# Optimization experiments

Measured on AMD Instinct MI355X. Metric: run time of the kernel, lower is better.

Reference implementation:

```python
import jax, jax.numpy as jnp
import numpy as np

N_HEADS = 12
HIDDEN = 768  # NOTE: d_head == hidden_size in this module (unusual)

def setup_inputs() -> dict:
    key = jax.random.key(0)
    ks = jax.random.split(key, 4)
    b, s = 8, 512
    d3 = 3 * N_HEADS * HIDDEN
    return {
        "x": jax.random.normal(ks[0], (b, s, HIDDEN), dtype=jnp.float32),
        "mask": jnp.zeros((b, 1, 1, s), dtype=jnp.float32),
        "w_qkv": jax.random.normal(ks[1], (d3, HIDDEN), dtype=jnp.float32) * 0.02,
        "b_qkv": jnp.zeros((d3,), dtype=jnp.float32),
        "w_o": jax.random.normal(ks[2], (HIDDEN, N_HEADS * HIDDEN), dtype=jnp.float32) * 0.02,
        "b_o": jnp.zeros((HIDDEN,), dtype=jnp.float32),
    }

def reference(x, mask, w_qkv, b_qkv, w_o, b_o):
    b, s, _ = x.shape
    nh = N_HEADS * HIDDEN
    qkv = x @ w_qkv.T + b_qkv                      # (b, s, 3*n*h)
    q, k, v = jnp.split(qkv, 3, axis=-1)           # each (b, s, n*h)
    def heads(t):
        return t.reshape(b, s, N_HEADS, HIDDEN).transpose(0, 2, 1, 3)  # (b, n, s, h)
    q, k, v = heads(q), heads(k), heads(v)
    scale = 1.0 / np.sqrt(HIDDEN).astype(np.float32)
    scores = jnp.einsum('bnqh,bnkh->bnqk', q, k) * scale  # (b, n, s_q, s_k)
    scores = scores + mask                         # additive mask broadcast
    a = jax.nn.softmax(scores, axis=-1)
    av = jnp.einsum('bnqk,bnkh->bnqh', a, v)       # (b, n, s, h)
    h = av.transpose(0, 2, 1, 3).reshape(b, s, nh) # (b, s, n*h)
    return h @ w_o.T + b_o                         # (b, s, hidden)
```

## Files before the change

### kernel.cpp

```cpp
#include <hip/hip_runtime.h>
#include <hip/hip_bf16.h>
#include <stdint.h>

#define AS1 __attribute__((address_space(1)))
#define AS3 __attribute__((address_space(3)))

typedef __attribute__((ext_vector_type(8))) __bf16 bf16x8;
typedef __attribute__((ext_vector_type(4))) float f32x4;
typedef unsigned short u16;
typedef __attribute__((ext_vector_type(8))) unsigned short u16x8;

#define B_    8
#define S_    512
#define NH_   12
#define HD_   768
#define NHD_  (NH_*HD_)
#define D3_   (3*NHD_)
#define QKLD_ (2*NHD_)
#define QK_SCALE 0.03608439182435161f

__device__ __forceinline__ u16 f2bf(float x) {
  union { float f; unsigned u; } a; a.f = x;
  unsigned r = a.u + 0x7fffu + ((a.u >> 16) & 1u);
  return (u16)(r >> 16);
}
__device__ __forceinline__ float bf2f(u16 x) {
  union { unsigned u; float f; } a; a.u = ((unsigned)x) << 16; return a.f;
}
__device__ __forceinline__ uint2 pack4(float a, float b, float c, float d) {
  uint2 r;
  asm("v_cvt_pk_bf16_f32 %0, %1, %2" : "=v"(r.x) : "v"(a), "v"(b));
  asm("v_cvt_pk_bf16_f32 %0, %1, %2" : "=v"(r.y) : "v"(c), "v"(d));
  return r;
}

__device__ __forceinline__ void gload16(const void* g, void* l) {
  __builtin_amdgcn_global_load_lds((const AS1 void*)g, (AS3 void*)l, 16, 0, 0);
}

struct GP {
  const u16* A;
  const u16* B;
  long sAb, sAn, sBb, sBn;
  void* o0; void* o2;
  const float* bias;
  int mMask, mShift, zPerX;
};

template<int MODE, int LDA, int LDB, int KK>
__global__ __launch_bounds__(256)
void gemm_bt(GP p) {
  __shared__ __align__(16) char smem[32768];
  const int tid  = threadIdx.x;
  const int wave = tid >> 6, lane = tid & 63;
  const int wr = wave >> 1, wc = wave & 1;

  int m_idx, n_idx, z;
  if constexpr (MODE == 0) {
    m_idx = blockIdx.y; n_idx = blockIdx.x; z = 0;
  } else {
    const int bid = blockIdx.x;
    const int xcd = bid & 7, loc = bid >> 3;
    if constexpr (MODE == 1) {
      int inner;
      if (p.zPerX) { inner = loc & 15; z = xcd * p.zPerX + (loc >> 4); }
      else         { inner = bid & 15; z = bid >> 4; }
      m_idx = inner >> 2; n_idx = inner & 3;
    } else if constexpr (MODE == 2) {
      int inner;
      if (p.zPerX) { inner = loc % 24; z = xcd * p.zPerX + loc / 24; }
      else         { inner = bid % 24; z = bid / 24; }
      m_idx = inner / 6; n_idx = inner - (inner / 6) * 6;
    } else {
      m_idx = loc & p.mMask;
      n_idx = (xcd & 1) * 3 + (loc >> p.mShift);
      z = xcd >> 1;
    }
  }
  const int bm0 = m_idx * 128, bn0 = n_idx * 128;
  const int zb  = z / NH_, zn = z - zb * NH_;

  const u16* A  = p.A + zb * p.sAb + zn * p.sAn;
  const u16* Bm = p.B + zb * p.sBb + zn * p.sBn;

  f32x4 acc[4][4];
  const f32x4 zero4 = {0.f, 0.f, 0.f, 0.f};
#pragma unroll
  for (int i = 0; i < 4; ++i)
#pragma unroll
    for (int j = 0; j < 4; ++j) acc[i][j] = zero4;

  const int scolsw = ((lane & 7) ^ (lane >> 3)) * 8;
  const u16* gA = A  + (size_t)(bm0 + wave*8 + (lane>>3)) * LDA + scolsw;
  const u16* gB = Bm + (size_t)(bn0 + wave*8 + (lane>>3)) * LDB + scolsw;
  char* ldsA = smem;
  char* ldsB = smem + 16384;
  char* stA  = ldsA + wave*1024;
  char* stB  = ldsB + wave*1024;

  const int aRow = (wr*64 + (lane&15)) * 128;
  const int bRow = (wc*64 + (lane&15)) * 128;
  const int csw  = lane & 7;
  const int cOff0 = (((lane>>4)    ) ^ csw) << 4;
  const int cOff1 = ((4 + (lane>>4)) ^ csw) << 4;

  for (int k0 = 0; k0 < KK; k0 += 64) {
#pragma unroll
    for (int i = 0; i < 4; ++i) {
      gload16(gA + (size_t)i*32*LDA, stA + i*4096);
      gload16(gB + (size_t)i*32*LDB, stB + i*4096);
    }
    gA += 64; gB += 64;
    __syncthreads();
#pragma unroll
    for (int kk = 0; kk < 2; ++kk) {
      const int cOff = kk ? cOff1 : cOff0;
      bf16x8 av[4], bv[4];
#pragma unroll
      for (int i = 0; i < 4; ++i)
        av[i] = *(const bf16x8*)(ldsA + aRow + i*2048 + cOff);
#pragma unroll
      for (int j = 0; j < 4; ++j)
        bv[j] = *(const bf16x8*)(ldsB + bRow + j*2048 + cOff);
#pragma unroll
      for (int i = 0; i < 4; ++i)
#pragma unroll
        for (int j = 0; j < 4; ++j)
          acc[i][j] = __builtin_amdgcn_mfma_f32_16x16x32_bf16(bv[j], av[i], acc[i][j], 0, 0, 0);
    }
    __syncthreads();
  }

  const int mBase = bm0 + wr*64 + (lane & 15);
  const int nBase = bn0 + wc*64 + ((lane >> 4) << 2);
#pragma unroll
  for (int i = 0; i < 4; ++i) {
    const int m = mBase + i*16;
#pragma unroll
    for (int j = 0; j < 4; ++j) {
      const int n = nBase + j*16;
      const f32x4 v = acc[i][j];
      if constexpr (MODE == 0) {
        const float4 b4 = *(const float4*)(p.bias + n);
        if (bn0 < QKLD_) {
          *(uint2*)((u16*)p.o0 + (long)m * QKLD_ + n) =
              pack4(v[0]+b4.x, v[1]+b4.y, v[2]+b4.z, v[3]+b4.w);
        } else {
          const int vcol = n - QKLD_;
          const int nh = vcol / HD_;
          const int h  = vcol - nh * HD_;
          u16* vb = (u16*)p.o2 + (long)((m >> 9) * NH_ + nh) * (S_*HD_)
                    + (long)h * S_ + (m & 511);
          vb[0]    = f2bf(v[0]+b4.x);
          vb[512]  = f2bf(v[1]+b4.y);
          vb[1024] = f2bf(v[2]+b4.z);
          vb[1536] = f2bf(v[3]+b4.w);
        }
      } else if constexpr (MODE == 1) {
        *(uint2*)((u16*)p.o0 + (long)z*S_*S_ + (long)m*S_ + n) =
            pack4(v[0]*QK_SCALE, v[1]*QK_SCALE, v[2]*QK_SCALE, v[3]*QK_SCALE);
      } else if constexpr (MODE == 2) {
        *(uint2*)((u16*)p.o0 + (long)(zb*S_ + m)*QKLD_ + zn*HD_ + n) =
            pack4(v[0], v[1], v[2], v[3]);
      } else {
        const long rowsTot = (long)(p.mMask + 1) * 128;
        *(float4*)((float*)p.o0 + ((long)z * rowsTot + m) * HD_ + n) =
            *(const float4*)&v;
      }
    }
  }
}

__global__ __launch_bounds__(256)
void softmax_rows(u16* __restrict__ SP, const float* __restrict__ maskc) {
  const int wave = threadIdx.x >> 6, lane = threadIdx.x & 63;
  const int rid = blockIdx.x * 4 + wave;
  const int z = rid >> 9;
  const int b = z / NH_;
  const u16x8 sv = *(const u16x8*)(SP + (size_t)rid * S_ + lane*8);
  const float* mrow = maskc + (size_t)b * S_;
  float vals[8];
  float m = -3.4e38f;
#pragma unroll
  for (int j = 0; j < 8; ++j) {
    vals[j] = bf2f(sv[j]) + mrow[lane*8 + j];
    m = fmaxf(m, vals[j]);
  }
#pragma unroll
  for (int o = 32; o > 0; o >>= 1) m = fmaxf(m, __shfl_xor(m, o));
  float sum = 0.f;
#pragma unroll
  for (int j = 0; j < 8; ++j) { vals[j] = __expf(vals[j] - m); sum += vals[j]; }
#pragma unroll
  for (int o = 32; o > 0; o >>= 1) sum += __shfl_xor(sum, o);
  const float inv = 1.0f / sum;
  u16x8 pv;
#pragma unroll
  for (int j = 0; j < 8; ++j) pv[j] = f2bf(vals[j] * inv);
  *(u16x8*)(SP + (size_t)rid * S_ + lane*8) = pv;
}

__global__ __launch_bounds__(256)
void cvt_bf16(const float4* __restrict__ in, ushort4* __restrict__ out, int n4) {
  const int i = blockIdx.x * 256 + threadIdx.x;
  if (i >= n4) return;
  const float4 v = in[i];
  ushort4 o;
  o.x = f2bf(v.x); o.y = f2bf(v.y); o.z = f2bf(v.z); o.w = f2bf(v.w);
  out[i] = o;
}

__global__ __launch_bounds__(256)
void combine_out(const float4* __restrict__ part, const float* __restrict__ b,
                 float4* __restrict__ out, int n4) {
  const int i = blockIdx.x * 256 + threadIdx.x;
  if (i >= n4) return;
  const float4 a0 = part[i];
  const float4 a1 = part[i + (size_t)n4];
  const float4 a2 = part[i + (size_t)2*n4];
  const float4 a3 = part[i + (size_t)3*n4];
  const int c = (i * 4) % HD_;
  float4 o;
  o.x = a0.x + a1.x + a2.x + a3.x + b[c];
  o.y = a0.y + a1.y + a2.y + a3.y + b[c+1];
  o.z = a0.z + a1.z + a2.z + a3.z + b[c+2];
  o.w = a0.w + a1.w + a2.w + a3.w + b[c+3];
  out[i] = o;
}

extern "C" void kernel_launch(void* const* d_in, const int* in_sizes, int n_in,
                              void* d_out, int out_size, void* d_ws, size_t ws_size,
                              hipStream_t stream) {
  const float* x     = (const float*)d_in[0];
  const float* mask  = (const float*)d_in[1];
  const float* w_qkv = (const float*)d_in[2];
  const float* b_qkv = (const float*)d_in[3];
  const float* w_o   = (const float*)d_in[4];
  const float* b_o   = (const float*)d_in[5];
  float* out = (float*)d_out;

  int bc = 0;
  for (int c = 8; c >= 1; c >>= 1)
    if (56623104UL + (unsigned long)c*35389440UL <= ws_size) { bc = c; break; }
  if (bc == 0) return;

  char* ws = (char*)d_ws;
  u16* wqb = (u16*)(ws);
  u16* wob = (u16*)(ws + 42467328L);
  u16* xb  = (u16*)(ws + 56623104L);
  long off = 56623104L + (long)bc*786432L;
  u16* QKn = (u16*)(ws + off);  off += (long)bc*18874368L;
  u16* Vt  = (u16*)(ws + off);  off += (long)bc*9437184L;
  u16* SP  = (u16*)(ws + off);
  u16* H   = QKn;
  float* Part = (float*)SP;

  cvt_bf16<<<dim3(D3_*HD_/4/256), dim3(256), 0, stream>>>((const float4*)w_qkv, (ushort4*)wqb, D3_*HD_/4);
  cvt_bf16<<<dim3(HD_*NHD_/4/256), dim3(256), 0, stream>>>((const float4*)w_o, (ushort4*)wob, HD_*NHD_/4);

  const int nchunks = B_ / bc;
  const int rows_c = bc * S_;
  const int zc = bc * NH_;
  const int mT = rows_c / 128;
  const int mShift = __builtin_ctz(mT);
  const int zPerX = (zc % 8 == 0) ? zc / 8 : 0;

  for (int c = 0; c < nchunks; ++c) {
    const long row0 = (long)c * rows_c;

    cvt_bf16<<<dim3(rows_c*HD_/4/256), dim3(256), 0, stream>>>(
        (const float4*)(x + row0*HD_), (ushort4*)xb, rows_c*HD_/4);

    GP p1; p1.A = xb; p1.B = wqb;
    p1.sAb = 0; p1.sAn = 0; p1.sBb = 0; p1.sBn = 0;
    p1.o0 = QKn; p1.o2 = Vt; p1.bias = b_qkv;
    p1.mMask = mT - 1; p1.mShift = mShift; p1.zPerX = 0;
    gemm_bt<0, HD_, HD_, HD_><<<dim3(216, mT, 1), dim3(256), 0, stream>>>(p1);

    GP p2; p2.A = QKn; p2.B = QKn + NHD_;
    p2.sAb = (long)S_*QKLD_; p2.sAn = HD_;
    p2.sBb = (long)S_*QKLD_; p2.sBn = HD_;
    p2.o0 = SP; p2.o2 = nullptr; p2.bias = nullptr;
    p2.mMask = 0; p2.mShift = 0; p2.zPerX = zPerX;
    gemm_bt<1, QKLD_, QKLD_, HD_><<<dim3(zc * 16), dim3(256), 0, stream>>>(p2);

    softmax_rows<<<dim3(zc*S_/4), dim3(256), 0, stream>>>(SP, mask + (long)c*bc*S_);

    GP p3; p3.A = SP; p3.B = Vt;
    p3.sAb = (long)NH_*S_*S_; p3.sAn = (long)S_*S_;
    p3.sBb = (long)NH_*S_*HD_; p3.sBn = (long)S_*HD_;
    p3.o0 = H; p3.o2 = nullptr; p3.bias = nullptr;
    p3.mMask = 0; p3.mShift = 0; p3.zPerX = zPerX;
    gemm_bt<2, S_, S_, S_><<<dim3(zc * 24), dim3(256), 0, stream>>>(p3);

    GP p4; p4.A = H; p4.B = wob;
    p4.sAb = 0; p4.sAn = NHD_/4;
    p4.sBb = 0; p4.sBn = NHD_/4;
    p4.o0 = Part; p4.o2 = nullptr; p4.bias = nullptr;
    p4.mMask = mT - 1; p4.mShift = mShift; p4.zPerX = 0;
    gemm_bt<3, QKLD_, NHD_, NHD_/4><<<dim3(24 * mT), dim3(256), 0, stream>>>(p4);

    combine_out<<<dim3(rows_c*HD_/4/256), dim3(256), 0, stream>>>(
        (const float4*)Part, b_o, (float4*)(out + row0*HD_), rows_c*HD_/4);
  }
}
```

Baseline: 526.0 us.

## Double-buffer LDS tiles with K=32 stages and prefetch next tile

Restructures the GEMM main loop to use two LDS buffers with a K-step of 32 instead of a single buffer with K-step 64. The next tile is loaded while the current one is computed, and partial vmcnt waits replace the full syncthreads. The LDS layout and swizzle change to 64-byte rows. This is meant to hide global-load latency behind MFMA work, at the cost of twice as many barriers per unit of K and less MFMA work per iteration.

```diff
diff --git a/kernel.cpp b/kernel.cpp
--- a/kernel.cpp
+++ b/kernel.cpp
@@ -90,45 +90,60 @@
 #pragma unroll
     for (int j = 0; j < 4; ++j) acc[i][j] = zero4;
 
-  const int scolsw = ((lane & 7) ^ (lane >> 3)) * 8;
-  const u16* gA = A  + (size_t)(bm0 + wave*8 + (lane>>3)) * LDA + scolsw;
-  const u16* gB = Bm + (size_t)(bn0 + wave*8 + (lane>>3)) * LDB + scolsw;
+  const int scolsw = ((lane & 3) ^ ((lane >> 3) & 3)) * 8;
+  const int srow = wave * 32 + (lane >> 2);
+  const u16* gA = A  + (size_t)(bm0 + srow) * LDA + scolsw;
+  const u16* gB = Bm + (size_t)(bn0 + srow) * LDB + scolsw;
+  const int stw = wave * 2048;
+
   char* ldsA = smem;
   char* ldsB = smem + 16384;
-  char* stA  = ldsA + wave*1024;
-  char* stB  = ldsB + wave*1024;
-
-  const int aRow = (wr*64 + (lane&15)) * 128;
-  const int bRow = (wc*64 + (lane&15)) * 128;
-  const int csw  = lane & 7;
-  const int cOff0 = (((lane>>4)    ) ^ csw) << 4;
-  const int cOff1 = ((4 + (lane>>4)) ^ csw) << 4;
-
-  for (int k0 = 0; k0 < KK; k0 += 64) {
-#pragma unroll
-    for (int i = 0; i < 4; ++i) {
-      gload16(gA + (size_t)i*32*LDA, stA + i*4096);
-      gload16(gB + (size_t)i*32*LDB, stB + i*4096);
+
+  auto stage = [&](int t) {
+    char* da = ldsA + (t & 1) * 8192 + stw;
+    char* db = ldsB + (t & 1) * 8192 + stw;
+    const u16* sa = gA + t * 32;
+    const u16* sb = gB + t * 32;
+    gload16(sa,                     da);
+    gload16(sa + (size_t)16 * LDA,  da + 1024);
+    gload16(sb,                     db);
+    gload16(sb + (size_t)16 * LDB,  db + 1024);
+  };
+
+  const int aRow = (wr * 64 + (lane & 15)) * 64;
+  const int bRow = (wc * 64 + (lane & 15)) * 64;
+  const int cOff = (((lane >> 4)) ^ ((lane >> 1) & 3)) << 4;
+
+  constexpr int NT = KK / 32;
+  stage(0);
+  for (int t = 0; t < NT; ++t) {
+    if (t + 1 < NT) {
+      stage(t + 1);
+      asm volatile("s_waitcnt vmcnt(4)" ::: "memory");
+    } else {
+      asm volatile("s_waitcnt vmcnt(0)" ::: "memory");
     }
-    gA += 64; gB += 64;
-    __syncthreads();
-#pragma unroll
-    for (int kk = 0; kk < 2; ++kk) {
-      const int cOff = kk ? cOff1 : cOff0;
-      bf16x8 av[4], bv[4];
-#pragma unroll
-      for (int i = 0; i < 4; ++i)
-        av[i] = *(const bf16x8*)(ldsA + aRow + i*2048 + cOff);
+    __builtin_amdgcn_s_barrier();
+    asm volatile("" ::: "memory");
+
+    const char* bA = ldsA + (t & 1) * 8192;
+    const char* bB = ldsB + (t & 1) * 8192;
+    bf16x8 av[4], bv[4];
+#pragma unroll
+    for (int i = 0; i < 4; ++i)
+      av[i] = *(const bf16x8*)(bA + aRow + i * 1024 + cOff);
+#pragma unroll
+    for (int j = 0; j < 4; ++j)
+      bv[j] = *(const bf16x8*)(bB + bRow + j * 1024 + cOff);
+#pragma unroll
+    for (int i = 0; i < 4; ++i)
 #pragma unroll
       for (int j = 0; j < 4; ++j)
-        bv[j] = *(const bf16x8*)(ldsB + bRow + j*2048 + cOff);
-#pragma unroll
-      for (int i = 0; i < 4; ++i)
-#pragma unroll
-        for (int j = 0; j < 4; ++j)
-          acc[i][j] = __builtin_amdgcn_mfma_f32_16x16x32_bf16(bv[j], av[i], acc[i][j], 0, 0, 0);
-    }
-    __syncthreads();
+        acc[i][j] = __builtin_amdgcn_mfma_f32_16x16x32_bf16(bv[j], av[i], acc[i][j], 0, 0, 0);
+
+    asm volatile("" ::: "memory");
+    __builtin_amdgcn_s_barrier();
+    asm volatile("" ::: "memory");
   }
 
   const int mBase = bm0 + wr*64 + (lane & 15);
```

Result: slower. 568.2 us (+8.0%).
